# Kernel optimization log

Measured on AMD Instinct MI355X. Metric: run time of the kernel, lower is better.

The kernel has to match this reference:

```python
import jax, jax.numpy as jnp
import numpy as np


def _cell(x, h, c, Wih, Whh, bih, bhh):
    # torch.nn.LSTMCell gate order: i, f, g, o
    gates = x @ Wih.T + h @ Whh.T + bih + bhh  # [B, 4H]
    i, f, g, o = jnp.split(gates, 4, axis=-1)
    i = jax.nn.sigmoid(i)
    f = jax.nn.sigmoid(f)
    g = jnp.tanh(g)
    o = jax.nn.sigmoid(o)
    c_new = f * c + i * g
    h_new = o * jnp.tanh(c_new)
    return h_new, c_new


def setup_inputs() -> dict:
    key = jax.random.key(0)
    B, T, D, H = 4096, 256, 4, 16
    ks = jax.random.split(key, 32)
    s = 1.0 / np.sqrt(H)  # torch LSTMCell/Linear uniform init bound

    def u(k, shape):
        return jax.random.uniform(k, shape, jnp.float32, -s, s)

    inp = {"y": jax.random.normal(ks[0], (B, T, D), jnp.float32)}
    names = ["f1", "f2", "f3", "b1", "b2", "b3"]
    ins = [D, H, H, D, H, H]
    idx = 1
    for n, di in zip(names, ins):
        inp[f"Wih_{n}"] = u(ks[idx], (4 * H, di)); idx += 1
        inp[f"Whh_{n}"] = u(ks[idx], (4 * H, H)); idx += 1
        inp[f"bih_{n}"] = u(ks[idx], (4 * H,)); idx += 1
        inp[f"bhh_{n}"] = u(ks[idx], (4 * H,)); idx += 1
    inp["W_out"] = u(ks[idx], (4, 2 * H)); idx += 1
    inp["b_out"] = u(ks[idx], (4,))
    return inp


def reference(y,
              Wih_f1, Whh_f1, bih_f1, bhh_f1,
              Wih_f2, Whh_f2, bih_f2, bhh_f2,
              Wih_f3, Whh_f3, bih_f3, bhh_f3,
              Wih_b1, Whh_b1, bih_b1, bhh_b1,
              Wih_b2, Whh_b2, bih_b2, bhh_b2,
              Wih_b3, Whh_b3, bih_b3, bhh_b3,
              W_out, b_out):
    B = y.shape[0]
    H = Whh_f1.shape[1]
    z = jnp.zeros((B, H), y.dtype)
    carry0 = (z, z, z, z, z, z, z, z, z, z, z, z)
    # forward-time and reversed-time sequences, time-major for scan: [T, B, 4]
    xs = (jnp.swapaxes(y, 0, 1), jnp.swapaxes(y[:, ::-1, :], 0, 1))

    def step(carry, x_t):
        hf1, cf1, hf2, cf2, hf3, cf3, hb1, cb1, hb2, cb2, hb3, cb3 = carry
        xf, xb = x_t
        hf1, cf1 = _cell(xf, hf1, cf1, Wih_f1, Whh_f1, bih_f1, bhh_f1)
        hf2, cf2 = _cell(hf1, hf2, cf2, Wih_f2, Whh_f2, bih_f2, bhh_f2)
        hf3, cf3 = _cell(hf2, hf3, cf3, Wih_f3, Whh_f3, bih_f3, bhh_f3)
        hb1, cb1 = _cell(xb, hb1, cb1, Wih_b1, Whh_b1, bih_b1, bhh_b1)
        hb2, cb2 = _cell(hb1, hb2, cb2, Wih_b2, Whh_b2, bih_b2, bhh_b2)
        hb3, cb3 = _cell(hb2, hb3, cb3, Wih_b3, Whh_b3, bih_b3, bhh_b3)
        return (hf1, cf1, hf2, cf2, hf3, cf3, hb1, cb1, hb2, cb2, hb3, cb3), None

    carry, _ = jax.lax.scan(step, carry0, xs)
    hf3, hb3 = carry[4], carry[10]
    out = jnp.concatenate([hf3, hb3], axis=1) @ W_out.T + b_out  # [B, 4]
    return out[:, None, :]  # [B, 1, 4]
```

## Files before the change

### kernel.cpp

```cpp
#include <hip/hip_runtime.h>

#define T_LEN 256
#define D_IN 4
#define NSTEP (T_LEN + 2)

typedef __fp16 h8 __attribute__((ext_vector_type(8)));
typedef __fp16 cvt2_t __attribute__((ext_vector_type(2)));
typedef float float4v __attribute__((ext_vector_type(4)));

struct CellW { const float *Wih, *Whh, *bih, *bhh; };
struct Params { CellW c[6]; const float* y; float* hout; };

__device__ __forceinline__ float fexp2(float x) { return __builtin_amdgcn_exp2f(x); }
__device__ __forceinline__ float frcp(float x)  { return __builtin_amdgcn_rcpf(x); }
__device__ __forceinline__ int packh(float a, float b) {
    cvt2_t p = __builtin_amdgcn_cvt_pkrtz(a, b);
    return __builtin_bit_cast(int, p);
}
__device__ __forceinline__ h8 mk8(int a, int b, int c, int d) {
    int4 v; v.x = a; v.y = b; v.z = c; v.w = d;
    return __builtin_bit_cast(h8, v);
}

#define MFMA32(a, b, c) __builtin_amdgcn_mfma_f32_16x16x32_f16(a, b, c, 0, 0, 0)

__device__ __forceinline__ void act2(const float4v& pA, const float4v& pB,
                                     float& cA, float& cB,
                                     float& hA, float& hB) {
    float eiA = fexp2(pA[0]), efA = fexp2(pA[1]), egA = fexp2(pA[2]);
    float eiB = fexp2(pB[0]), efB = fexp2(pB[1]), egB = fexp2(pB[2]);
    float FA = 1.f + efA,              FB = 1.f + efB;
    float PA = (1.f + eiA) * (1.f + egA), PB = (1.f + eiB) * (1.f + egB);
    float NGA = 1.f - egA,             NGB = 1.f - egB;
    float denA = FA * PA,              denB = FB * PB;
    float numA = fmaf(cA, PA, NGA * FA);
    float numB = fmaf(cB, PB, NGB * FB);
    float RC = frcp(denA * denB);
    cA = numA * denB * RC;
    cB = numB * denA * RC;
    const float K2 = -2.8853900817779268f;
    float eoA = fexp2(pA[3]), ecA = fexp2(fminf(cA * K2, 30.f));
    float eoB = fexp2(pB[3]), ecB = fexp2(fminf(cB * K2, 30.f));
    float NOA = 1.f - ecA,    NOB = 1.f - ecB;
    float DhA = (1.f + eoA) * (1.f + ecA);
    float DhB = (1.f + eoB) * (1.f + ecB);
    float RH = frcp(DhA * DhB);
    hA = NOA * DhB * RH;
    hB = NOB * DhA * RH;
}

__global__ void __launch_bounds__(768)
__attribute__((amdgpu_waves_per_eu(3, 4)))
lstm_wf_kernel(Params p)
{
    __shared__ int2 x_lds[2][T_LEN][16];
    __shared__ int h_pk[2][2][3][2][4][16];
    __shared__ int pad_excl[3072];

    const int tid = threadIdx.x;
    const int v = tid >> 6;
    const int half = (v >= 6);
    const int v6 = v - 6 * half;
    const int l = v6 >> 1;
    const int e = v6 & 1;
    const int L = tid & 63;
    const int n = L & 15;
    const int Q = L >> 4;

    const int b0 = blockIdx.x * 16;
    const CellW cw = p.c[half * 3 + l];
    const float LOG2E = 1.4426950408889634f;

    if (tid == 767) pad_excl[0] = tid;

    for (int i = tid; i < 2 * 2 * 3 * 2 * 4 * 16; i += 768)
        ((int*)h_pk)[i] = 0;
    for (int i = tid; i < 2 * T_LEN * 16; i += 768) {
        const int d = i >> 12;
        const int r = i & 4095;
        const int t = r >> 4, nn = r & 15;
        const int tt = d ? (T_LEN - 1 - t) : t;
        const float4 xv = *(const float4*)(p.y +
            ((size_t)(b0 + nn) * T_LEN + tt) * D_IN);
        int2 xp; xp.x = packh(xv.x, xv.y); xp.y = packh(xv.z, xv.w);
        x_lds[d][t][nn] = xp;
    }

    const int gate = n & 3;
    const int su = n >> 2;
    const float sA = (gate == 2) ? -2.f * LOG2E : -LOG2E;
    h8 A8[2];
    float4v bs[2];
#pragma unroll
    for (int j = 0; j < 2; ++j) {
        const int u = 8 * e + 4 * j + su;
        const int row = gate * 16 + u;
        float vh[4], vp[4];
#pragma unroll
        for (int i = 0; i < 4; ++i) {
            const int col = 4 * i + Q;
            vh[i] = cw.Whh[row * 16 + col];
            vp[i] = (l == 0) ? ((Q == 0) ? cw.Wih[row * D_IN + i] : 0.f)
                             : cw.Wih[row * 16 + col];
        }
        A8[j] = mk8(packh(vh[0] * sA, vh[1] * sA), packh(vh[2] * sA, vh[3] * sA),
                    packh(vp[0] * sA, vp[1] * sA), packh(vp[2] * sA, vp[3] * sA));
        const int ub = 8 * e + 4 * j + Q;
        const float br0 = cw.bih[0 * 16 + ub] + cw.bhh[0 * 16 + ub];
        const float br1 = cw.bih[1 * 16 + ub] + cw.bhh[1 * 16 + ub];
        const float br2 = cw.bih[2 * 16 + ub] + cw.bhh[2 * 16 + ub];
        const float br3 = cw.bih[3 * 16 + ub] + cw.bhh[3 * 16 + ub];
        bs[j] = (float4v){br0 * -LOG2E, br1 * -LOG2E,
                          br2 * -2.f * LOG2E, br3 * -LOG2E};
    }

    __syncthreads();

    float cA = 0.f, cB = 0.f;
    float hA = 0.f, hB = 0.f;

#pragma unroll 1
    for (int s = 0; s < NSTEP; ++s) {
        if (s >= l && s - l < T_LEN) {
            const int t = s - l;
            const int pr = (s + 1) & 1;
            const int* hsO = &h_pk[half][pr][l][0][Q][n];
            const int o0 = hsO[0];
            const int o1 = hsO[64];
            int pd0, pd1;
            if (l == 0) {
                const int2 xv = x_lds[half][t][n];
                pd0 = (Q == 0) ? xv.x : 0;
                pd1 = (Q == 0) ? xv.y : 0;
            } else {
                const int* hsP = &h_pk[half][pr][l - 1][0][Q][n];
                pd0 = hsP[0];
                pd1 = hsP[64];
            }
            const h8 b8 = mk8(o0, o1, pd0, pd1);
            float4v p0 = MFMA32(A8[0], b8, bs[0]);
            float4v p1 = MFMA32(A8[1], b8, bs[1]);
            act2(p0, p1, cA, cB, hA, hB);
            const int pw = s & 1;
            h_pk[half][pw][l][e][Q][n] = packh(hA, hB);
        }
        __syncthreads();
    }

    if (l == 2) {
        float* o = p.hout + (size_t)(b0 + n) * 32 + half * 16;
        o[8 * e + Q]     = hA;
        o[8 * e + 4 + Q] = hB;
    }
}

__global__ void out_proj_kernel(const float* __restrict__ ws,
                                const float* __restrict__ Wout,
                                const float* __restrict__ bout,
                                float* __restrict__ out, int B)
{
    int idx = blockIdx.x * blockDim.x + threadIdx.x;
    if (idx >= B * 4) return;
    int b = idx >> 2, o = idx & 3;
    float acc = bout[o];
    const float* h = ws + (size_t)b * 32;
    const float* w = Wout + o * 32;
#pragma unroll
    for (int m = 0; m < 32; ++m) acc = fmaf(h[m], w[m], acc);
    out[idx] = acc;
}

extern "C" void kernel_launch(void* const* d_in, const int* in_sizes, int n_in,
                              void* d_out, int out_size, void* d_ws, size_t ws_size,
                              hipStream_t stream)
{
    const int B = in_sizes[0] / (T_LEN * D_IN);

    Params p;
    for (int s = 0; s < 6; ++s) {
        p.c[s].Wih = (const float*)d_in[1 + 4 * s];
        p.c[s].Whh = (const float*)d_in[2 + 4 * s];
        p.c[s].bih = (const float*)d_in[3 + 4 * s];
        p.c[s].bhh = (const float*)d_in[4 + 4 * s];
    }
    p.y = (const float*)d_in[0];
    p.hout = (float*)d_ws;

    const int blocks = B / 16;
    lstm_wf_kernel<<<blocks, 768, 0, stream>>>(p);

    const float* Wout = (const float*)d_in[25];
    const float* bout = (const float*)d_in[26];
    out_proj_kernel<<<(B * 4 + 255) / 256, 256, 0, stream>>>(
        (const float*)d_ws, Wout, bout, (float*)d_out, B);
}
```

Baseline: 243.2 us.

## Stream inputs into registers and peel wavefront prologue/epilogue steps

Replaces the upfront staging of the whole input sequence in LDS with per-step global loads that prefetch two timesteps ahead into registers. Each wave keeps its own packed h in a register and reads only its sibling's half from LDS. The loop is unrolled by two with the prologue and epilogue steps peeled, so buffer indices and active flags become compile-time constants. LDS padding is enlarged to keep occupancy the same, which could add global-load latency to each serial step.

```diff
diff --git a/kernel.cpp b/kernel.cpp
--- a/kernel.cpp
+++ b/kernel.cpp
@@ -2,7 +2,6 @@
 
 #define T_LEN 256
 #define D_IN 4
-#define NSTEP (T_LEN + 2)
 
 typedef __fp16 h8 __attribute__((ext_vector_type(8)));
 typedef __fp16 cvt2_t __attribute__((ext_vector_type(2)));
@@ -53,14 +52,13 @@
 __attribute__((amdgpu_waves_per_eu(3, 4)))
 lstm_wf_kernel(Params p)
 {
-    __shared__ int2 x_lds[2][T_LEN][16];
-    __shared__ int h_pk[2][2][3][2][4][16];
-    __shared__ int pad_excl[3072];
+    __shared__ int h_sl[2][2][2][3][4][16];
+    __shared__ int pad_excl[19456];
 
     const int tid = threadIdx.x;
     const int v = tid >> 6;
-    const int half = (v >= 6);
-    const int v6 = v - 6 * half;
+    const int dir = (v >= 6);
+    const int v6 = v - 6 * dir;
     const int l = v6 >> 1;
     const int e = v6 & 1;
     const int L = tid & 63;
@@ -68,23 +66,13 @@
     const int Q = L >> 4;
 
     const int b0 = blockIdx.x * 16;
-    const CellW cw = p.c[half * 3 + l];
+    const CellW cw = p.c[dir * 3 + l];
     const float LOG2E = 1.4426950408889634f;
 
     if (tid == 767) pad_excl[0] = tid;
 
-    for (int i = tid; i < 2 * 2 * 3 * 2 * 4 * 16; i += 768)
-        ((int*)h_pk)[i] = 0;
-    for (int i = tid; i < 2 * T_LEN * 16; i += 768) {
-        const int d = i >> 12;
-        const int r = i & 4095;
-        const int t = r >> 4, nn = r & 15;
-        const int tt = d ? (T_LEN - 1 - t) : t;
-        const float4 xv = *(const float4*)(p.y +
-            ((size_t)(b0 + nn) * T_LEN + tt) * D_IN);
-        int2 xp; xp.x = packh(xv.x, xv.y); xp.y = packh(xv.z, xv.w);
-        x_lds[d][t][nn] = xp;
-    }
+    for (int i = tid; i < 2 * 2 * 2 * 3 * 4 * 16; i += 768)
+        ((int*)h_sl)[i] = 0;
 
     const int gate = n & 3;
     const int su = n >> 2;
@@ -114,41 +102,71 @@
                           br2 * -2.f * LOG2E, br3 * -LOG2E};
     }
 
+    const float* ybase = p.y + (size_t)(b0 + n) * (T_LEN * D_IN);
+    int2 xr0 = {0, 0}, xr1 = {0, 0};
+    if (l == 0 && L < 16) {
+        const int ta = dir ? (T_LEN - 1) : 0;
+        const int tb = dir ? (T_LEN - 2) : 1;
+        const float4 xa = *(const float4*)(ybase + (size_t)ta * D_IN);
+        const float4 xb = *(const float4*)(ybase + (size_t)tb * D_IN);
+        xr0.x = packh(xa.x, xa.y); xr0.y = packh(xa.z, xa.w);
+        xr1.x = packh(xb.x, xb.y); xr1.y = packh(xb.z, xb.w);
+    }
+
     __syncthreads();
 
     float cA = 0.f, cB = 0.f;
     float hA = 0.f, hB = 0.f;
-
-#pragma unroll 1
-    for (int s = 0; s < NSTEP; ++s) {
-        if (s >= l && s - l < T_LEN) {
-            const int t = s - l;
-            const int pr = (s + 1) & 1;
-            const int* hsO = &h_pk[half][pr][l][0][Q][n];
-            const int o0 = hsO[0];
-            const int o1 = hsO[64];
-            int pd0, pd1;
+    int ownpk = 0;
+
+    auto STEP = [&](int s, int pr, int pw, bool a0, bool a1, bool a2,
+                    int2& xr) {
+        const bool act = (l == 0) ? a0 : (l == 1) ? a1 : a2;
+        if (act) {
+            const int sib = h_sl[pr][dir][1 - e][l][Q][n];
+            int pv0, pv1;
             if (l == 0) {
-                const int2 xv = x_lds[half][t][n];
-                pd0 = (Q == 0) ? xv.x : 0;
-                pd1 = (Q == 0) ? xv.y : 0;
+                pv0 = (Q == 0) ? xr.x : 0;
+                pv1 = (Q == 0) ? xr.y : 0;
             } else {
-                const int* hsP = &h_pk[half][pr][l - 1][0][Q][n];
-                pd0 = hsP[0];
-                pd1 = hsP[64];
+                pv0 = h_sl[pr][dir][0][l - 1][Q][n];
+                pv1 = h_sl[pr][dir][1][l - 1][Q][n];
             }
-            const h8 b8 = mk8(o0, o1, pd0, pd1);
+            const int pk0 = e ? sib : ownpk;
+            const int pk1 = e ? ownpk : sib;
+            const h8 b8 = mk8(pk0, pk1, pv0, pv1);
             float4v p0 = MFMA32(A8[0], b8, bs[0]);
             float4v p1 = MFMA32(A8[1], b8, bs[1]);
             act2(p0, p1, cA, cB, hA, hB);
-            const int pw = s & 1;
-            h_pk[half][pw][l][e][Q][n] = packh(hA, hB);
+            ownpk = packh(hA, hB);
+            h_sl[pw][dir][e][l][Q][n] = ownpk;
+            if (l == 0 && L < 16) {
+                const int t2 = s + 2;
+                if (t2 < T_LEN) {
+                    const int tt = dir ? (T_LEN - 1 - t2) : t2;
+                    const float4 xv = *(const float4*)(ybase + (size_t)tt * D_IN);
+                    xr.x = packh(xv.x, xv.y);
+                    xr.y = packh(xv.z, xv.w);
+                }
+            }
         }
         __syncthreads();
-    }
+    };
+
+    STEP(0, 1, 0, true, false, false, xr0);
+    STEP(1, 0, 1, true, true, false, xr1);
+
+#pragma unroll 1
+    for (int s = 2; s < T_LEN; s += 2) {
+        STEP(s,     1, 0, true, true, true, xr0);
+        STEP(s + 1, 0, 1, true, true, true, xr1);
+    }
+
+    STEP(256, 1, 0, false, true, true, xr0);
+    STEP(257, 0, 1, false, false, true, xr1);
 
     if (l == 2) {
-        float* o = p.hout + (size_t)(b0 + n) * 32 + half * 16;
+        float* o = p.hout + (size_t)(b0 + n) * 32 + dir * 16;
         o[8 * e + Q]     = hA;
         o[8 * e + 4 + Q] = hB;
     }
```

New measurement: 230.4 us. 1.06x faster.
